# Kernel tuning notes

Hardware: AMD Instinct MI355X
Metric: run time of the kernel (lower is better)

## Reference

```python
import jax, jax.numpy as jnp
import numpy as np

NB = 10          # number_of_basis (hardcoded in module)
MAX_RADIUS = 3.5
DIM_SH = 16      # spherical harmonics l = 0..3 -> (3+1)^2 components


def spherical_harmonics_l3(vec):
    # real spherical harmonics l=0..3 of the normalized vector,
    # 'component' normalization (each component has unit variance on S^2)
    r = jnp.sqrt(jnp.sum(vec * vec, -1, keepdims=True))
    u = vec / jnp.maximum(r, 1e-9)
    x, y, z = u[..., 0], u[..., 1], u[..., 2]
    s3, s5, s15 = jnp.sqrt(3.0), jnp.sqrt(5.0), jnp.sqrt(15.0)
    c358 = jnp.sqrt(35.0 / 8.0); c218 = jnp.sqrt(21.0 / 8.0)
    sh = [jnp.ones_like(x),
          s3 * x, s3 * y, s3 * z,
          s15 * x * y, s15 * y * z, (s5 / 2) * (3 * z * z - 1),
          s15 * x * z, (s15 / 2) * (x * x - y * y),
          c358 * y * (3 * x * x - y * y), jnp.sqrt(105.0) * x * y * z,
          c218 * y * (5 * z * z - 1), (jnp.sqrt(7.0) / 2) * z * (5 * z * z - 3),
          c218 * x * (5 * z * z - 1), (jnp.sqrt(105.0) / 2) * z * (x * x - y * y),
          c358 * x * (x * x - 3 * y * y)]
    return jnp.stack(sh, -1)  # [E, 16]


def soft_one_hot(r):
    # e3nn soft_one_hot_linspace, basis='smooth_finite', cutoff=True
    values = jnp.linspace(0.0, MAX_RADIUS, NB + 2)[1:-1]
    step = MAX_RADIUS / (NB + 1)
    u = (r[:, None] - values) / step
    mask = jnp.abs(u) < 1.0
    us = jnp.where(mask, u, 0.0)
    y = jnp.where(mask, jnp.exp(-1.0 / (1.0 - us * us)), 0.0)
    return 1.14136 * jnp.exp(2.0) * y * jnp.sqrt(float(NB))  # * number_of_basis**0.5


def soft_unit_step(t):
    ts = jnp.where(t > 0, t, 1.0)
    return jnp.where(t > 0, jnp.exp(-1.0 / ts), 0.0)


def fcnet(e, W1, W2):
    # e3nn FullyConnectedNet([10, 16, weight_numel], act=silu): bias-free,
    # fan-in normalized linear layers
    h = jax.nn.silu(e @ W1 / jnp.sqrt(float(e.shape[-1])))
    return h @ W2 / jnp.sqrt(float(W1.shape[-1]))


def setup_inputs() -> dict:
    key = jax.random.key(0)
    ks = jax.random.split(key, 9)
    N, E, C, DK = 20000, 50000, 16, 8
    pos = jax.random.uniform(ks[0], (N, 3), jnp.float32) * 2.0  # box so most edges < max_radius
    x = jax.random.normal(ks[1], (N, C), jnp.float32)
    Wq = jax.random.normal(ks[2], (C, DK), jnp.float32)
    Wk1 = jax.random.normal(ks[3], (NB, 16), jnp.float32)
    Wk2 = jax.random.normal(ks[4], (16, C * DIM_SH * DK), jnp.float32)
    Wv1 = jax.random.normal(ks[5], (NB, 16), jnp.float32)
    Wv2 = jax.random.normal(ks[6], (16, C * DIM_SH * DK), jnp.float32)
    edge_src = jax.random.randint(ks[7], (E,), 0, N, jnp.int32)
    edge_dst = jax.random.randint(ks[8], (E,), 0, N, jnp.int32)
    return {"pos": pos, "x": x, "Wq": Wq, "Wk1": Wk1, "Wk2": Wk2,
            "Wv1": Wv1, "Wv2": Wv2, "edge_src": edge_src, "edge_dst": edge_dst}


def reference(pos, x, Wq, Wk1, Wk2, Wv1, Wv2, edge_src, edge_dst):
    N, C = x.shape
    E = edge_src.shape[0]
    DK = Wq.shape[1]
    edge_vec = pos[edge_src] - pos[edge_dst]                    # [E, 3]
    r = jnp.sqrt(jnp.sum(edge_vec * edge_vec, -1) + 1e-18)      # [E]
    emb = soft_one_hot(r)                                       # [E, 10]
    cutoff = soft_unit_step(10.0 * (1.0 - r / MAX_RADIUS))      # [E]
    sh = spherical_harmonics_l3(edge_vec)                       # [E, 16]
    # per-edge weight-conditioned tensor products (shared_weights=False)
    wk = fcnet(emb, Wk1, Wk2).reshape(E, C, DIM_SH, DK)
    wv = fcnet(emb, Wv1, Wv2).reshape(E, C, DIM_SH, DK)
    xs = x[edge_src]                                            # gather [E, C]
    norm = jnp.sqrt(float(C * DIM_SH))
    k = jnp.einsum('ec,ej,ecjo->eo', xs, sh, wk) / norm         # [E, DK]
    v = jnp.einsum('ec,ej,ecjo->eo', xs, sh, wv) / norm         # [E, DK]
    q = x @ Wq                                                  # [N, DK]
    logits = jnp.sum(q[edge_dst] * k, -1) / jnp.sqrt(float(DK)) # [E]
    expv = cutoff * jnp.exp(logits)
    z = jax.ops.segment_sum(expv, edge_dst, num_segments=N)     # segment-softmax denom
    z = jnp.where(z == 0.0, 1.0, z)
    alpha = expv / z[edge_dst]
    w = jnp.sqrt(jax.nn.relu(alpha))
    out = jax.ops.segment_sum(w[:, None] * v, edge_dst, num_segments=N)  # [N, DK]
    return out
```

## Files before the change

kernel.cpp:

```cpp
#include <hip/hip_runtime.h>
#include <hip/hip_bf16.h>

#define NBASIS 10
#define CDIM 16
#define DKDIM 8
#define JDIM 16

typedef _Float16 half8 __attribute__((ext_vector_type(8)));
typedef float floatx4 __attribute__((ext_vector_type(4)));

__device__ __forceinline__ float ldf(const void* p, int i, int f32) {
    if (f32) return ((const float*)p)[i];
    return __bfloat162float(((const __hip_bfloat16*)p)[i]);
}

__device__ __forceinline__ int detect_f32(const void* x) {
    unsigned short b = ((const unsigned short*)x)[threadIdx.x & 63];
    float v = __uint_as_float(((unsigned int)b) << 16);
    bool bad = !(fabsf(v) < 1000.0f) || (v != 0.0f && fabsf(v) < 1e-15f);
    unsigned long long m = __ballot(bad);
    return (__popcll(m) >= 8) ? 1 : 0;
}

__device__ __forceinline__ const float* uniform_ptr(const float* p) {
    uint64_t v = (uint64_t)p;
    uint32_t lo = __builtin_amdgcn_readfirstlane((uint32_t)v);
    uint32_t hi = __builtin_amdgcn_readfirstlane((uint32_t)(v >> 32));
    return (const float*)(((uint64_t)hi << 32) | lo);
}

__global__ __launch_bounds__(256) void prep_kernel(
    const void* __restrict__ x, const void* __restrict__ Wq,
    const void* __restrict__ Wk1, const void* __restrict__ Wk2,
    const void* __restrict__ Wv1, const void* __restrict__ Wv2,
    float* __restrict__ w1k, float* __restrict__ w1v,
    float* __restrict__ qbuf, float* __restrict__ zbuf,
    float* __restrict__ outacc, _Float16* __restrict__ Bpk, int N)
{
    const int f32 = detect_f32(x);
    int i = blockIdx.x * 256 + threadIdx.x;
    if (i < 160) { w1k[i] = ldf(Wk1, i, f32); w1v[i] = ldf(Wv1, i, f32); }
    if (i < 65536) {
        int j = i & 7, lane = (i >> 3) & 63, ks = (i >> 9) & 7, nt = i >> 12;
        int kk = ks * 32 + (lane >> 4) * 8 + j;
        int nn = nt * 16 + (lane & 15);
        int c = kk >> 4, jj = kk & 15;
        int net = nn >> 7, m = (nn >> 3) & 15, o = nn & 7;
        float v = ldf(net ? Wv2 : Wk2, m * 2048 + c * 128 + jj * 8 + o, f32);
        Bpk[i] = (_Float16)v;
    }
    if (i < N) zbuf[i] = 0.0f;
    if (i < N * 8) {
        outacc[i] = 0.0f;
        int n = i >> 3, o = i & 7;
        float acc = 0.0f;
        #pragma unroll
        for (int c = 0; c < CDIM; ++c)
            acc = fmaf(ldf(x, n * CDIM + c, f32), ldf(Wq, c * DKDIM + o, f32), acc);
        qbuf[i] = acc;
    }
}

__global__ __launch_bounds__(256) void edge_kernel(
    const void* __restrict__ pos, const void* __restrict__ x,
    const int* __restrict__ esrc, const int* __restrict__ edst,
    const float* __restrict__ w1k, const float* __restrict__ w1v,
    const float* __restrict__ qbuf, const _Float16* __restrict__ Bpk,
    float* __restrict__ zbuf, float* __restrict__ outacc, int E)
{
    __shared__ union {
        struct { float xs[64][17]; float sh[64][17]; } g;
        _Float16 A[16384];
        struct { float pk[2][64][9]; float pv[2][64][9]; } p;
    } u;
    __shared__ _Float16 hm_lds[64][34];
    __shared__ float cut_lds[64];
    __shared__ float evs_lds[64];
    __shared__ int   d_lds[64];

    const int f32  = detect_f32(x);
    const int tid  = threadIdx.x;
    const int lane = tid & 63;
    const int w    = tid >> 6;
    const int q    = lane >> 4;
    const int e0   = blockIdx.x * 64;
    const int e_g  = e0 + lane;
    const int eidx = (e_g < E) ? e_g : (E - 1);
    const int s = esrc[eidx], d = edst[eidx];

    float vx = ldf(pos, s * 3 + 0, f32) - ldf(pos, d * 3 + 0, f32);
    float vy = ldf(pos, s * 3 + 1, f32) - ldf(pos, d * 3 + 1, f32);
    float vz = ldf(pos, s * 3 + 2, f32) - ldf(pos, d * 3 + 2, f32);
    float r2 = vx * vx + vy * vy + vz * vz;
    float r  = sqrtf(r2 + 1e-18f);

    if (w == 0) {
        float rsh = sqrtf(r2);
        float inv = 1.0f / fmaxf(rsh, 1e-9f);
        float ux = vx * inv, uy = vy * inv, uz = vz * inv;
        const float s3   = 1.7320508075688772f;
        const float s5   = 2.23606797749979f;
        const float s15  = 3.872983346207417f;
        const float c358 = 2.091650066335189f;
        const float c218 = 1.6201851746019651f;
        const float s105 = 10.246950765959598f;
        const float s7h  = 1.3228756555322954f;
        float xx = ux * ux, yy = uy * uy, zz = uz * uz;
        float sh[16];
        sh[0] = 1.0f;
        sh[1] = s3 * ux; sh[2] = s3 * uy; sh[3] = s3 * uz;
        sh[4] = s15 * ux * uy;
        sh[5] = s15 * uy * uz;
        sh[6] = 0.5f * s5 * (3.0f * zz - 1.0f);
        sh[7] = s15 * ux * uz;
        sh[8] = 0.5f * s15 * (xx - yy);
        sh[9] = c358 * uy * (3.0f * xx - yy);
        sh[10] = s105 * ux * uy * uz;
        sh[11] = c218 * uy * (5.0f * zz - 1.0f);
        sh[12] = s7h * uz * (5.0f * zz - 3.0f);
        sh[13] = c218 * ux * (5.0f * zz - 1.0f);
        sh[14] = 0.5f * s105 * uz * (xx - yy);
        sh[15] = c358 * ux * (xx - 3.0f * yy);
        #pragma unroll
        for (int j = 0; j < 16; ++j) u.g.sh[lane][j] = sh[j];
        float tcut = 10.0f * (1.0f - r * (1.0f / 3.5f));
        cut_lds[lane] = (tcut > 0.0f) ? expf(-1.0f / tcut) : 0.0f;
        d_lds[lane] = d;
    } else if (w == 1) {
        #pragma unroll
        for (int c = 0; c < CDIM; ++c)
            u.g.xs[lane][c] = ldf(x, s * CDIM + c, f32);
    } else {
        const float* w1 = uniform_ptr((w == 2) ? w1k : w1v);
        const int off = (w == 2) ? 0 : 16;
        float emb[NBASIS];
        const float step = 3.5f / 11.0f;
        const float istep = 11.0f / 3.5f;
        const float coef = (float)(1.14136 * 7.38905609893065 * 3.1622776601683795);
        #pragma unroll
        for (int i = 0; i < NBASIS; ++i) {
            float uu = (r - step * (float)(i + 1)) * istep; uu *= uu;
            emb[i] = (uu < 1.0f) ? coef * expf(-1.0f / (1.0f - uu)) : 0.0f;
        }
        const float inv_s10 = 0.31622776601683794f;
        #pragma unroll
        for (int m = 0; m < 16; ++m) {
            float pre = 0.0f;
            #pragma unroll
            for (int nb = 0; nb < NBASIS; ++nb)
                pre = fmaf(emb[nb], w1[nb * 16 + m], pre);
            pre *= inv_s10;
            hm_lds[lane][off + m] = (_Float16)(pre / (1.0f + expf(-pre)));
        }
    }
    __syncthreads();

    half8 af[8];
    {
        const int erow = w * 16 + (lane & 15);
        const int coff = q >> 1, jj0 = (q & 1) * 8;
        #pragma unroll
        for (int ks = 0; ks < 8; ++ks) {
            float xsv = u.g.xs[erow][ks * 2 + coff];
            half8 a;
            #pragma unroll
            for (int j = 0; j < 8; ++j)
                a[j] = (_Float16)(xsv * u.g.sh[erow][jj0 + j]);
            af[ks] = a;
        }
    }
    __syncthreads();
    {
        half8* Af = (half8*)u.A;
        #pragma unroll
        for (int ks = 0; ks < 8; ++ks)
            Af[(w * 8 + ks) * 64 + lane] = af[ks];
    }
    __syncthreads();

    float part[16];
    #pragma unroll
    for (int i = 0; i < 16; ++i) part[i] = 0.0f;
    const int b3   = (lane >> 3) & 1;
    const int moff = (w >> 1) * 16;
    const half8* Af = (const half8*)u.A;
    const half8* Bf = (const half8*)Bpk;

    #pragma unroll
    for (int rp = 0; rp < 2; ++rp) {
        half8 a0[8], a1[8];
        #pragma unroll
        for (int ks = 0; ks < 8; ++ks) {
            a0[ks] = Af[((2 * rp)     * 8 + ks) * 64 + lane];
            a1[ks] = Af[((2 * rp + 1) * 8 + ks) * 64 + lane];
        }
        floatx4 acc0[4], acc1[4];
        #pragma unroll
        for (int l = 0; l < 4; ++l) {
            acc0[l] = (floatx4){0.f, 0.f, 0.f, 0.f};
            acc1[l] = (floatx4){0.f, 0.f, 0.f, 0.f};
        }
        #pragma unroll
        for (int l = 0; l < 4; ++l) {
            const int nt = 4 * w + l;
            #pragma unroll
            for (int ks = 0; ks < 8; ++ks) {
                half8 b = Bf[(nt * 8 + ks) * 64 + lane];
                acc0[l] = __builtin_amdgcn_mfma_f32_16x16x32_f16(a0[ks], b, acc0[l], 0, 0, 0);
                acc1[l] = __builtin_amdgcn_mfma_f32_16x16x32_f16(a1[ks], b, acc1[l], 0, 0, 0);
            }
        }
        #pragma unroll
        for (int l = 0; l < 4; ++l) {
            const int m = ((4 * w + l) * 2 + b3) & 15;
            #pragma unroll
            for (int rr = 0; rr < 4; ++rr) {
                const int er = q * 4 + rr;
                part[(2 * rp) * 4 + rr] +=
                    (float)hm_lds[(2 * rp) * 16 + er][moff + m] * acc0[l][rr];
                part[(2 * rp + 1) * 4 + rr] +=
                    (float)hm_lds[(2 * rp + 1) * 16 + er][moff + m] * acc1[l][rr];
            }
        }
    }
    #pragma unroll
    for (int i = 0; i < 16; ++i) part[i] += __shfl_xor(part[i], 8, 64);

    __syncthreads();
    if (b3 == 0) {
        const int o = lane & 7;
        #pragma unroll
        for (int i = 0; i < 16; ++i) {
            const int e = (i >> 2) * 16 + q * 4 + (i & 3);
            if (w < 2) u.p.pk[w][e][o] = part[i];
            else       u.p.pv[w - 2][e][o] = part[i];
        }
    }
    __syncthreads();

    if (tid < 64) {
        const int dd = d_lds[tid];
        float logit = 0.0f;
        #pragma unroll
        for (int o = 0; o < 8; ++o) {
            float kv = u.p.pk[0][tid][o] + u.p.pk[1][tid][o];
            logit = fmaf(qbuf[(size_t)dd * 8 + o], kv, logit);
        }
        logit *= (1.0f / 64.0f) * 0.35355339059327373f;
        float ev = cut_lds[tid] * expf(logit);
        if (e0 + tid < E) atomicAdd(&zbuf[dd], ev);
        evs_lds[tid] = sqrtf(ev);
    }
    __syncthreads();

    {
        const int el = tid & 63, op = tid >> 6;
        if (e0 + el < E) {
            const int dd = d_lds[el];
            const float wq = evs_lds[el] * (1.0f / 64.0f);
            float v0 = u.p.pv[0][el][2 * op]     + u.p.pv[1][el][2 * op];
            float v1 = u.p.pv[0][el][2 * op + 1] + u.p.pv[1][el][2 * op + 1];
            atomicAdd(&outacc[(size_t)dd * 8 + 2 * op],     wq * v0);
            atomicAdd(&outacc[(size_t)dd * 8 + 2 * op + 1], wq * v1);
        }
    }
}

__global__ __launch_bounds__(256) void finalize_kernel(
    const float* __restrict__ outacc, const float* __restrict__ zbuf,
    void* __restrict__ out, const void* __restrict__ x, int n)
{
    const int f32 = detect_f32(x);
    int i = blockIdx.x * 256 + threadIdx.x;
    if (i < n) {
        float z = zbuf[i >> 3];
        z = (z == 0.0f) ? 1.0f : z;
        float val = outacc[i] / sqrtf(z);
        if (f32) ((float*)out)[i] = val;
        else ((__hip_bfloat16*)out)[i] = __float2bfloat16(val);
    }
}

extern "C" void kernel_launch(void* const* d_in, const int* in_sizes, int n_in,
                              void* d_out, int out_size, void* d_ws, size_t ws_size,
                              hipStream_t stream)
{
    const void* pos = d_in[0];
    const void* x   = d_in[1];
    const void* Wq  = d_in[2];
    const void* Wk1 = d_in[3];
    const void* Wk2 = d_in[4];
    const void* Wv1 = d_in[5];
    const void* Wv2 = d_in[6];
    const int* esrc = (const int*)d_in[7];
    const int* edst = (const int*)d_in[8];
    const int N = in_sizes[1] / CDIM;
    const int E = in_sizes[7];

    float* ws = (float*)d_ws;
    float* w1k    = ws;
    float* w1v    = w1k + 160;
    float* qbuf   = w1v + 160;
    float* zbuf   = qbuf + (size_t)N * 8;
    float* outacc = zbuf + N;
    _Float16* Bpk = (_Float16*)(outacc + (size_t)N * 8);

    int prep_threads = N * 8 > 65536 ? N * 8 : 65536;
    int prep_blocks = (prep_threads + 255) / 256;
    prep_kernel<<<prep_blocks, 256, 0, stream>>>(x, Wq, Wk1, Wk2, Wv1, Wv2,
                                                 w1k, w1v, qbuf, zbuf, outacc,
                                                 Bpk, N);

    int edge_blocks = (E + 63) / 64;
    edge_kernel<<<edge_blocks, 256, 0, stream>>>(pos, x, esrc, edst,
                                                 w1k, w1v, qbuf, Bpk,
                                                 zbuf, outacc, E);

    finalize_kernel<<<(N * 8 + 255) / 256, 256, 0, stream>>>(
        outacc, zbuf, d_out, x, N * 8);
}
```

Baseline: 113.9 us.

## Replace float atomic scatter with per-node linked lists and gather reduction

The edge kernel no longer does float atomicAdds into z and output accumulators. Instead it builds a per-destination linked list using atomicExch on a head array, stores per-edge exp values and fp16 value vectors, and a node kernel walks each list twice to compute the softmax denominator and the weighted sum. This removes contended float atomics (about 9 per edge) but adds pointer-chasing, serial dependent loads in the node kernel, and fp16 rounding of v.

```diff
diff --git a/kernel.cpp b/kernel.cpp
--- a/kernel.cpp
+++ b/kernel.cpp
@@ -34,8 +34,8 @@
     const void* __restrict__ Wk1, const void* __restrict__ Wk2,
     const void* __restrict__ Wv1, const void* __restrict__ Wv2,
     float* __restrict__ w1k, float* __restrict__ w1v,
-    float* __restrict__ qbuf, float* __restrict__ zbuf,
-    float* __restrict__ outacc, _Float16* __restrict__ Bpk, int N)
+    float* __restrict__ qbuf, _Float16* __restrict__ Bpk,
+    int* __restrict__ head, int N)
 {
     const int f32 = detect_f32(x);
     int i = blockIdx.x * 256 + threadIdx.x;
@@ -49,9 +49,8 @@
         float v = ldf(net ? Wv2 : Wk2, m * 2048 + c * 128 + jj * 8 + o, f32);
         Bpk[i] = (_Float16)v;
     }
-    if (i < N) zbuf[i] = 0.0f;
+    if (i < N) head[i] = -1;
     if (i < N * 8) {
-        outacc[i] = 0.0f;
         int n = i >> 3, o = i & 7;
         float acc = 0.0f;
         #pragma unroll
@@ -66,7 +65,8 @@
     const int* __restrict__ esrc, const int* __restrict__ edst,
     const float* __restrict__ w1k, const float* __restrict__ w1v,
     const float* __restrict__ qbuf, const _Float16* __restrict__ Bpk,
-    float* __restrict__ zbuf, float* __restrict__ outacc, int E)
+    int* __restrict__ head, int* __restrict__ next,
+    float* __restrict__ evb, _Float16* __restrict__ vbuf, int E)
 {
     __shared__ union {
         struct { float xs[64][17]; float sh[64][17]; } g;
@@ -75,7 +75,6 @@
     } u;
     __shared__ _Float16 hm_lds[64][34];
     __shared__ float cut_lds[64];
-    __shared__ float evs_lds[64];
     __shared__ int   d_lds[64];
 
     const int f32  = detect_f32(x);
@@ -87,6 +86,9 @@
     const int e_g  = e0 + lane;
     const int eidx = (e_g < E) ? e_g : (E - 1);
     const int s = esrc[eidx], d = edst[eidx];
+
+    int prev = -1;
+    if (w == 0 && e_g < E) prev = atomicExch(&head[d], e_g);
 
     float vx = ldf(pos, s * 3 + 0, f32) - ldf(pos, d * 3 + 0, f32);
     float vy = ldf(pos, s * 3 + 1, f32) - ldf(pos, d * 3 + 1, f32);
@@ -176,6 +178,7 @@
         for (int ks = 0; ks < 8; ++ks)
             Af[(w * 8 + ks) * 64 + lane] = af[ks];
     }
+    if (w == 0 && e_g < E) next[e_g] = prev;
     __syncthreads();
 
     float part[16];
@@ -247,38 +250,39 @@
             logit = fmaf(qbuf[(size_t)dd * 8 + o], kv, logit);
         }
         logit *= (1.0f / 64.0f) * 0.35355339059327373f;
-        float ev = cut_lds[tid] * expf(logit);
-        if (e0 + tid < E) atomicAdd(&zbuf[dd], ev);
-        evs_lds[tid] = sqrtf(ev);
-    }
-    __syncthreads();
+        if (e0 + tid < E)
+            evb[e0 + tid] = cut_lds[tid] * expf(logit);
+    }
 
     {
         const int el = tid & 63, op = tid >> 6;
         if (e0 + el < E) {
-            const int dd = d_lds[el];
-            const float wq = evs_lds[el] * (1.0f / 64.0f);
             float v0 = u.p.pv[0][el][2 * op]     + u.p.pv[1][el][2 * op];
             float v1 = u.p.pv[0][el][2 * op + 1] + u.p.pv[1][el][2 * op + 1];
-            atomicAdd(&outacc[(size_t)dd * 8 + 2 * op],     wq * v0);
-            atomicAdd(&outacc[(size_t)dd * 8 + 2 * op + 1], wq * v1);
-        }
-    }
-}
-
-__global__ __launch_bounds__(256) void finalize_kernel(
-    const float* __restrict__ outacc, const float* __restrict__ zbuf,
-    void* __restrict__ out, const void* __restrict__ x, int n)
+            vbuf[(size_t)(e0 + el) * 8 + 2 * op]     = (_Float16)(v0 * (1.0f / 64.0f));
+            vbuf[(size_t)(e0 + el) * 8 + 2 * op + 1] = (_Float16)(v1 * (1.0f / 64.0f));
+        }
+    }
+}
+
+__global__ __launch_bounds__(256) void node_kernel(
+    const float* __restrict__ evb, const _Float16* __restrict__ vbuf,
+    const int* __restrict__ head, const int* __restrict__ next,
+    void* __restrict__ out, const void* __restrict__ x, int n8)
 {
     const int f32 = detect_f32(x);
     int i = blockIdx.x * 256 + threadIdx.x;
-    if (i < n) {
-        float z = zbuf[i >> 3];
-        z = (z == 0.0f) ? 1.0f : z;
-        float val = outacc[i] / sqrtf(z);
-        if (f32) ((float*)out)[i] = val;
-        else ((__hip_bfloat16*)out)[i] = __float2bfloat16(val);
-    }
+    if (i >= n8) return;
+    const int n = i >> 3, o = i & 7;
+    float z = 0.0f;
+    for (int e = head[n]; e >= 0; e = next[e]) z += evb[e];
+    z = (z == 0.0f) ? 1.0f : z;
+    const float invz = 1.0f / z;
+    float acc = 0.0f;
+    for (int e = head[n]; e >= 0; e = next[e])
+        acc += sqrtf(evb[e] * invz) * (float)vbuf[(size_t)e * 8 + o];
+    if (f32) ((float*)out)[i] = acc;
+    else ((__hip_bfloat16*)out)[i] = __float2bfloat16(acc);
 }
 
 extern "C" void kernel_launch(void* const* d_in, const int* in_sizes, int n_in,
@@ -297,25 +301,25 @@
     const int N = in_sizes[1] / CDIM;
     const int E = in_sizes[7];
 
-    float* ws = (float*)d_ws;
-    float* w1k    = ws;
-    float* w1v    = w1k + 160;
-    float* qbuf   = w1v + 160;
-    float* zbuf   = qbuf + (size_t)N * 8;
-    float* outacc = zbuf + N;
-    _Float16* Bpk = (_Float16*)(outacc + (size_t)N * 8);
+    _Float16* Bpk = (_Float16*)d_ws;
+    float* w1k  = (float*)(Bpk + 65536);
+    float* w1v  = w1k + 160;
+    float* qbuf = w1v + 160;
+    float* evb  = qbuf + (size_t)N * 8;
+    _Float16* vbuf = (_Float16*)(evb + E);
+    int*   head = (int*)(vbuf + (size_t)E * 8);
+    int*   next = head + N;
 
     int prep_threads = N * 8 > 65536 ? N * 8 : 65536;
     int prep_blocks = (prep_threads + 255) / 256;
     prep_kernel<<<prep_blocks, 256, 0, stream>>>(x, Wq, Wk1, Wk2, Wv1, Wv2,
-                                                 w1k, w1v, qbuf, zbuf, outacc,
-                                                 Bpk, N);
+                                                 w1k, w1v, qbuf, Bpk, head, N);
 
     int edge_blocks = (E + 63) / 64;
     edge_kernel<<<edge_blocks, 256, 0, stream>>>(pos, x, esrc, edst,
                                                  w1k, w1v, qbuf, Bpk,
-                                                 zbuf, outacc, E);
-
-    finalize_kernel<<<(N * 8 + 255) / 256, 256, 0, stream>>>(
-        outacc, zbuf, d_out, x, N * 8);
-}
+                                                 head, next, evb, vbuf, E);
+
+    node_kernel<<<(N * 8 + 255) / 256, 256, 0, stream>>>(
+        evb, vbuf, head, next, d_out, x, N * 8);
+}
```

Result: faster. 101.4 us (-11.0%).
